# Kernel optimization log

Measured on AMD Instinct MI355X. Metric: run time of the kernel, lower is better.

The kernel has to match this reference:

```python
import jax, jax.numpy as jnp
import numpy as np
import math

HID, NH, DH = 512, 4, 128
H, W = 30, 54
N = H * W          # 1620 tokens
MEM, B = 2, 1
NG = 4             # temporal groups
L = (H // 2) * (W // 2)  # 405
FF = 4 * HID


def _ln(x, g, b, eps=1e-5):
    m = x.mean(-1, keepdims=True)
    v = ((x - m) ** 2).mean(-1, keepdims=True)
    return (x - m) / jnp.sqrt(v + eps) * g + b


def setup_inputs() -> dict:
    key = jax.random.key(0)
    ks = jax.random.split(key, 24)
    w = lambda k, s: (jax.random.normal(k, s, jnp.float32) * 0.02)
    return {
        'x': jax.random.normal(ks[0], (B, N, HID), jnp.float32),
        'memory': jax.random.normal(ks[1], (MEM, N, HID), jnp.float32),
        # spatial block params (weights stored as (in, out) so y = x @ W + b)
        's_g1': jnp.ones(HID), 's_b1': jnp.zeros(HID),
        's_wq': w(ks[2], (HID, HID)), 's_bq': jnp.zeros(HID),
        's_wk': w(ks[3], (HID, HID)), 's_bk': jnp.zeros(HID),
        's_wv': w(ks[4], (HID, HID)), 's_bv': jnp.zeros(HID),
        's_wo': w(ks[5], (HID, HID)), 's_bo': jnp.zeros(HID),
        's_g2': jnp.ones(HID), 's_b2': jnp.zeros(HID),
        's_w1': w(ks[6], (HID, FF)), 's_fb1': jnp.zeros(FF),
        's_w2': w(ks[7], (FF, HID)), 's_fb2': jnp.zeros(HID),
        # temporal block params (forward only uses norm2 + ffn)
        't_g2': jnp.ones(HID), 't_b2': jnp.zeros(HID),
        't_w1': w(ks[8], (HID, FF)), 't_fb1': jnp.zeros(FF),
        't_w2': w(ks[9], (FF, HID)), 't_fb2': jnp.zeros(HID),
    }


def _spatial_block(x, memory, g1, b1, wq, bq, wk, bk, wv, bv, wo, bo, g2, b2, w1, fb1, w2, fb2):
    xc = jnp.concatenate([x, memory], axis=0)          # (t, n, hid), t = B + MEM
    t = xc.shape[0]
    xn = _ln(xc, g1, b1)
    q = (xn @ wq + bq).reshape(t, N, NH, DH).transpose(0, 2, 1, 3)
    k = (xn @ wk + bk).reshape(t, N, NH, DH).transpose(0, 2, 1, 3)
    v = (xn @ wv + bv).reshape(t, N, NH, DH).transpose(0, 2, 1, 3)
    scores = jnp.einsum('thqd,thkd->thqk', q, k) / math.sqrt(DH)
    probs = jax.nn.softmax(scores, axis=-1)
    o = jnp.einsum('thqk,thkd->thqd', probs, v).transpose(0, 2, 1, 3).reshape(t, N, HID)
    o = o @ wo + bo
    xu = xc + o
    y = _ln(xu, g2, b2)
    xa = xu + (jax.nn.relu(y @ w1 + fb1) @ w2 + fb2)
    return xa[:B], jnp.concatenate([memory[1:], x], axis=0)


def _temporal_block(x, memory, g2, b2, w1, fb1, w2, fb2):
    xc = jnp.concatenate([x, memory], axis=0)          # (t, n, hid)
    t = xc.shape[0]
    # (t, 2, h/2, 2, w/2, NH, DH) -> (t, 2, 2, NH, h/2, w/2, DH) -> (t, NG, NH, L, DH)
    xg = xc.reshape(t, 2, H // 2, 2, W // 2, NH, DH)
    xg = xg.transpose(0, 1, 3, 5, 2, 4, 6).reshape(t, NG, NH, L, DH)
    # Original code runs SDPA over all t but keeps only slice [-1]; since Q is
    # broadcast across t, attn_out[-1] == attention(Q, K[-1], V[-1]) exactly.
    q = xg[-1]                                          # (NG, NH, L, DH); K = V = q
    scores = jnp.einsum('gnld,gnmd->gnlm', q, q) / math.sqrt(DH)
    probs = jax.nn.softmax(scores, axis=-1)
    o = jnp.einsum('gnlm,gnmd->gnld', probs, q)         # (NG, NH, L, DH)
    o = o.transpose(0, 2, 1, 3).reshape(NG, L, HID)
    o = o.mean(axis=0, keepdims=True)                   # (1, L, HID)
    x_att = jnp.tile(o, (1, NG, 1))                     # (1, n, HID)
    xu = x + x_att
    y = _ln(xu, g2, b2)
    x_fin = xu + (jax.nn.relu(y @ w1 + fb1) @ w2 + fb2)
    return x_fin, jnp.concatenate([memory[1:], x], axis=0)


def reference(x, memory, s_g1, s_b1, s_wq, s_bq, s_wk, s_bk, s_wv, s_bv, s_wo, s_bo,
              s_g2, s_b2, s_w1, s_fb1, s_w2, s_fb2, t_g2, t_b2, t_w1, t_fb1, t_w2, t_fb2):
    x_sp, mem_sp = _spatial_block(x, memory, s_g1, s_b1, s_wq, s_bq, s_wk, s_bk,
                                  s_wv, s_bv, s_wo, s_bo, s_g2, s_b2, s_w1, s_fb1, s_w2, s_fb2)
    x_fin, mem_fin = _temporal_block(x_sp, mem_sp, t_g2, t_b2, t_w1, t_fb1, t_w2, t_fb2)
    return x_fin, mem_fin
```

## Files before the change

kernel.cpp:

```cpp
#include <hip/hip_runtime.h>
#include <stdint.h>

typedef unsigned short u16;
typedef float f32x4 __attribute__((ext_vector_type(4)));
typedef short s16x8 __attribute__((ext_vector_type(8)));

#define DEV __device__ __forceinline__

DEV float b2f(u16 u){ union{unsigned i; float f;} v; v.i = ((unsigned)u)<<16; return v.f; }
DEV u16 f2b(float f){ union{float f; unsigned i;} v; v.f=f; unsigned u=v.i;
                      return (u16)((u + 0x7FFFu + ((u>>16)&1u))>>16); }
DEV s16x8 ld8(const u16* p){ return *(const s16x8*)p; }

#define MFMA(d,a,b) d = __builtin_amdgcn_mfma_f32_16x16x32_bf16(a, b, d, 0, 0, 0)

DEV void gload16(const u16* g, u16* l){
  __builtin_amdgcn_global_load_lds((const __attribute__((address_space(1))) void*)g,
                                   (__attribute__((address_space(3))) void*)l, 16, 0, 0);
}

__global__ __launch_bounds__(64) void detect_kernel(const u16* __restrict__ x, int* flag){
  int lane = threadIdx.x;
  int cnt = 0;
  for (int i=0;i<32;i++){
    u16 v = x[lane*32+i];
    int e = (v >> 7) & 0xFF;
    if (e >= 0xE0) cnt++;
  }
  for (int off=1; off<64; off<<=1) cnt += __shfl_xor(cnt, off, 64);
  if (lane==0) *flag = (cnt >= 16) ? 1 : 0;
}

struct NormArgs { const void* src[15]; int cumblk[16]; };

__global__ __launch_bounds__(64) void norm_kernel(NormArgs a, const int* __restrict__ flag,
                                                  u16* __restrict__ canon){
  int b = blockIdx.x, lane = threadIdx.x;
  int t = 0;
  while (t < 14 && b >= a.cumblk[t+1]) t++;
  int off = (b - a.cumblk[t])*512 + lane*8;
  size_t g = (size_t)b*512 + lane*8;
  if (*flag){
    const float* s = (const float*)a.src[t] + off;
    s16x8 o;
#pragma unroll
    for (int j=0;j<8;j++) o[j] = (short)f2b(s[j]);
    *(s16x8*)(canon+g) = o;
  } else {
    *(s16x8*)(canon+g) = *(const s16x8*)((const u16*)a.src[t] + off);
  }
}

struct TJobs {
  const void* src[8]; u16* dst[8];
  int R[8], C32[8], srcld[8], dstld[8];
  int cum[9];
};
__global__ void trans_kernel(TJobs J, const int* __restrict__ flag){
  int b = blockIdx.x;
  int t = 0;
  while (b >= J.cum[t+1]) t++;
  int idx = b - J.cum[t];
  int tr = idx / J.C32[t], tc = idx - tr*J.C32[t];
  int r0 = tr*32, c0 = tc*32;
  const void* src = J.src[t];
  u16* dst = J.dst[t];
  int R = J.R[t], srcld = J.srcld[t], dstld = J.dstld[t];
  int isf32 = flag ? *flag : 0;
  __shared__ u16 tile[32][33];
  int tx = threadIdx.x, ty = threadIdx.y;
#pragma unroll
  for (int i=0;i<4;i++){
    int r = r0 + ty + i*8, c = c0 + tx;
    u16 v = 0;
    if (r < R){
      size_t si = (size_t)r*srcld + c;
      v = isf32 ? f2b(((const float*)src)[si]) : ((const u16*)src)[si];
    }
    tile[ty+i*8][tx] = v;
  }
  __syncthreads();
#pragma unroll
  for (int i=0;i<4;i++){
    int c = c0 + ty + i*8, r = r0 + tx;
    if (r < dstld) dst[(size_t)c*dstld + r] = tile[tx][ty+i*8];
  }
}

__global__ __launch_bounds__(256) void gemm_s_kernel(
    const u16* __restrict__ A, const u16* __restrict__ BT,
    const u16* __restrict__ bias, const u16* __restrict__ bias2, const u16* __restrict__ bias3,
    int M, int N, int K, int KS, float* __restrict__ pout,
    const u16* __restrict__ resid_bf, const float* __restrict__ resid_f,
    u16* __restrict__ out_bf, float* __restrict__ out_f,
    const int* __restrict__ flagp, u16* __restrict__ dev_bf, float* __restrict__ dev_f,
    int relu)
{
  __shared__ u16 Al[2][64*64];
  __shared__ u16 Bl[2][64*64];
  int tid = threadIdx.x, lane = tid & 63, w = tid >> 6;
  int lr = lane & 15, lk = lane >> 4;
  int wr = w >> 1, wc = w & 1;
  int rowBase = blockIdx.y*64, colBase = blockIdx.x*64;
  int z = blockIdx.z;
  int kStep = K / KS;
  int kOff = kStep * z;
  int nk = kStep >> 6;

  f32x4 acc[2][2] = {{{0,0,0,0},{0,0,0,0}},{{0,0,0,0},{0,0,0,0}}};

  auto STAGE = [&](int buf, int kt){
    int kb = kOff + kt*64;
#pragma unroll
    for (int it=0; it<2; ++it){
      int ch  = it*256 + tid;
      int row = ch >> 3, seg = ch & 7;
      int sseg = (seg ^ (row & 7)) << 3;
      int ar = min(rowBase + row, M-1);
      gload16(A  + (size_t)ar*K + kb + sseg, Al[buf] + ch*8);
      int bc = colBase + row;
      gload16(BT + (size_t)bc*K + kb + sseg, Bl[buf] + ch*8);
    }
  };

  STAGE(0, 0);
  asm volatile("s_waitcnt vmcnt(0)" ::: "memory");
  __syncthreads();
  int cur = 0;
  for (int kt=0; kt<nk; ++kt){
    if (kt+1 < nk) STAGE(cur^1, kt+1);
#pragma unroll
    for (int ks=0; ks<2; ++ks){
      s16x8 af[2], bf[2];
#pragma unroll
      for (int m=0;m<2;m++){
        int ar = wr*32 + m*16 + lr;
        af[m] = *(const s16x8*)(Al[cur] + ar*64 + ((((ks<<2)+lk) ^ (ar&7))<<3));
        int bc = wc*32 + m*16 + lr;
        bf[m] = *(const s16x8*)(Bl[cur] + bc*64 + ((((ks<<2)+lk) ^ (bc&7))<<3));
      }
#pragma unroll
      for (int m=0;m<2;m++)
#pragma unroll
        for (int n=0;n<2;n++) MFMA(acc[m][n], af[m], bf[n]);
    }
    asm volatile("s_waitcnt vmcnt(0)" ::: "memory");
    __syncthreads();
    cur ^= 1;
  }

  if (pout){
    float* pz = pout + (size_t)z*M*N;
#pragma unroll
    for (int m=0;m<2;m++)
#pragma unroll
      for (int n=0;n<2;n++){
        int col = colBase + wc*32 + n*16 + lr;
#pragma unroll
        for (int r=0;r<4;r++){
          int row = rowBase + wr*32 + m*16 + lk*4 + r;
          if (row < M) pz[(size_t)row*N + col] = acc[m][n][r];
        }
      }
    return;
  }
  int isf32 = flagp ? *flagp : 0;
#pragma unroll
  for (int m=0;m<2;m++){
#pragma unroll
    for (int n=0;n<2;n++){
      int col = colBase + wc*32 + n*16 + lr;
      float bv = 0.f;
      if (bias){
        if (bias2){
          const u16* bp = (col < 512) ? bias : ((col < 1024) ? bias2 : bias3);
          bv = b2f(bp[col & 511]);
        } else bv = b2f(bias[col]);
      }
#pragma unroll
      for (int r=0;r<4;r++){
        int row = rowBase + wr*32 + m*16 + lk*4 + r;
        if (row < M){
          float v = acc[m][n][r] + bv;
          if (relu) v = fmaxf(v, 0.f);
          size_t idx = (size_t)row*N + col;
          if (resid_bf) v += b2f(resid_bf[idx]);
          if (resid_f)  v += resid_f[idx];
          if (out_f)  out_f[idx]  = v;
          if (out_bf) out_bf[idx] = f2b(v);
          if (flagp){ if (isf32) dev_f[idx] = v; else dev_bf[idx] = f2b(v); }
        }
      }
    }
  }
}

__global__ __launch_bounds__(256) void gemm_comb_kernel(
    const float* __restrict__ pout, int KS, const u16* __restrict__ bias,
    int M, int relu,
    const u16* __restrict__ resid_bf, const float* __restrict__ resid_f,
    u16* __restrict__ out_bf, float* __restrict__ out_f,
    const int* __restrict__ flagp, u16* __restrict__ dev_bf, float* __restrict__ dev_f)
{
  int w = threadIdx.x >> 6, lane = threadIdx.x & 63;
  int row = blockIdx.x*4 + w;
  if (row >= M) return;
  int c0 = lane*8;
  float acc[8];
  const float* p0 = pout + (size_t)row*512 + c0;
#pragma unroll
  for (int j=0;j<8;j++) acc[j] = p0[j];
  for (int z=1; z<KS; ++z){
    const float* pz = pout + ((size_t)z*M + row)*512 + c0;
#pragma unroll
    for (int j=0;j<8;j++) acc[j] += pz[j];
  }
  int isf32 = flagp ? *flagp : 0;
#pragma unroll
  for (int j=0;j<8;j++){
    int col = c0 + j;
    float v = acc[j] + (bias ? b2f(bias[col]) : 0.f);
    if (relu) v = fmaxf(v, 0.f);
    size_t idx = (size_t)row*512 + col;
    if (resid_bf) v += b2f(resid_bf[idx]);
    if (resid_f)  v += resid_f[idx];
    if (out_f)  out_f[idx]  = v;
    if (out_bf) out_bf[idx] = f2b(v);
    if (flagp){ if (isf32) dev_f[idx] = v; else dev_bf[idx] = f2b(v); }
  }
}

__global__ __launch_bounds__(256) void comb_ln_kernel(
    const float* __restrict__ pout, int KS, const u16* __restrict__ bias, int M,
    const u16* __restrict__ resid_bf,
    float* __restrict__ out_f,
    const u16* __restrict__ gw, const u16* __restrict__ bw,
    u16* __restrict__ out_ln)
{
  int w = threadIdx.x >> 6, lane = threadIdx.x & 63;
  int row = blockIdx.x*4 + w;
  if (row >= M) return;
  int c0 = lane*8;
  float acc[8];
  const float* p0 = pout + (size_t)row*512 + c0;
#pragma unroll
  for (int j=0;j<8;j++) acc[j] = p0[j];
  for (int z=1; z<KS; ++z){
    const float* pz = pout + ((size_t)z*M + row)*512 + c0;
#pragma unroll
    for (int j=0;j<8;j++) acc[j] += pz[j];
  }
  float s = 0.f;
#pragma unroll
  for (int j=0;j<8;j++){
    acc[j] += b2f(bias[c0+j]) + b2f(resid_bf[(size_t)row*512 + c0 + j]);
    out_f[(size_t)row*512 + c0 + j] = acc[j];
    s += acc[j];
  }
#pragma unroll
  for (int off=1; off<64; off<<=1) s += __shfl_xor(s, off, 64);
  float mean = s*(1.f/512.f);
  float vs = 0.f;
#pragma unroll
  for (int j=0;j<8;j++){ float d = acc[j]-mean; vs += d*d; }
#pragma unroll
  for (int off=1; off<64; off<<=1) vs += __shfl_xor(vs, off, 64);
  float rstd = 1.f/sqrtf(vs*(1.f/512.f) + 1e-5f);
#pragma unroll
  for (int j=0;j<8;j++){
    int c = c0+j;
    out_ln[(size_t)row*512 + c] = f2b((acc[j]-mean)*rstd*b2f(gw[c]) + b2f(bw[c]));
  }
}

__global__ __launch_bounds__(256) void combine_ln_kernel(
    const float* __restrict__ xa0, const float* __restrict__ ot,
    float* __restrict__ xut,
    const u16* __restrict__ gw, const u16* __restrict__ bw,
    u16* __restrict__ out_ln)
{
  int w = threadIdx.x >> 6, lane = threadIdx.x & 63;
  int row = blockIdx.x*4 + w;
  int l = row % 405;
  int c0 = lane*8;
  const float* pa = xa0 + (size_t)row*512 + c0;
  float acc[8];
#pragma unroll
  for (int j=0;j<8;j++) acc[j] = pa[j];
#pragma unroll
  for (int g2=0; g2<4; ++g2){
    const float* po = ot + ((size_t)(g2*405+l))*512 + c0;
#pragma unroll
    for (int j=0;j<8;j++) acc[j] += 0.25f*po[j];
  }
  float s = 0.f;
#pragma unroll
  for (int j=0;j<8;j++){ xut[(size_t)row*512 + c0 + j] = acc[j]; s += acc[j]; }
#pragma unroll
  for (int off=1; off<64; off<<=1) s += __shfl_xor(s, off, 64);
  float mean = s*(1.f/512.f);
  float vs = 0.f;
#pragma unroll
  for (int j=0;j<8;j++){ float d = acc[j]-mean; vs += d*d; }
#pragma unroll
  for (int off=1; off<64; off<<=1) vs += __shfl_xor(vs, off, 64);
  float rstd = 1.f/sqrtf(vs*(1.f/512.f) + 1e-5f);
#pragma unroll
  for (int j=0;j<8;j++){
    int c = c0+j;
    out_ln[(size_t)row*512 + c] = f2b((acc[j]-mean)*rstd*b2f(gw[c]) + b2f(bw[c]));
  }
}

__global__ __launch_bounds__(256) void flash4_kernel(
    const u16* __restrict__ Qp, const u16* __restrict__ Kp, const u16* __restrict__ VTp,
    float* __restrict__ po, float* __restrict__ pm, float* __restrict__ pl,
    int M, int Nk, int qld, int tiles_total, int nchunks,
    long q_hi_stride, long vt_hi_stride, int vt_ld, float scale)
{
  int u = blockIdx.y, c = blockIdx.z;
  int uh = u >> 2, ul = u & 3;
  const u16* q  = Qp  + (size_t)uh*q_hi_stride + ul*128;
  const u16* kk = Kp  + (size_t)uh*q_hi_stride + ul*128;
  const u16* vt = VTp + (size_t)uh*vt_hi_stride + (size_t)(ul*128)*vt_ld;
  int tid = threadIdx.x, lane = tid & 63, w = tid >> 6;
  int lr = lane & 15, lk = lane >> 4;
  int r0 = blockIdx.x*64 + w*16;
  int qr = min(r0 + lr, M-1);

  __shared__ u16 Klds[64*128];
  __shared__ u16 Vlds[128*64];
  __shared__ u16 plsm[4][16*80];

  s16x8 qf[4];
#pragma unroll
  for (int kd=0; kd<4; ++kd) qf[kd] = ld8(q + (size_t)qr*qld + kd*32 + lk*8);
  f32x4 oacc[8];
#pragma unroll
  for (int i=0;i<8;i++) oacc[i] = (f32x4){0,0,0,0};
  float mr[4] = {-1e30f,-1e30f,-1e30f,-1e30f};
  float ls[4] = {0,0,0,0};

  int t0 = (tiles_total * c) / nchunks;
  int t1 = (tiles_total * (c+1)) / nchunks;
  for (int kt=t0; kt<t1; ++kt){
    int kb = kt*64;
#pragma unroll
    for (int it=0; it<4; ++it){
      int ch = it*256 + tid;
      int key = ch >> 4, seg = ch & 15;
      int kg = min(kb + key, Nk-1);
      s16x8 kvv = ld8(kk + (size_t)kg*qld + seg*8);
      int dd = ch >> 3, sg = ch & 7;
      s16x8 vvv = ld8(vt + (size_t)dd*vt_ld + kb + sg*8);
      *(s16x8*)(Klds + key*128 + ((seg*8) ^ ((key&7)<<3))) = kvv;
      *(s16x8*)(Vlds + dd*64  + ((sg*8)  ^ ((dd&7)<<3)))  = vvv;
    }
    __syncthreads();
    f32x4 s[4];
#pragma unroll
    for (int n=0;n<4;n++) s[n] = (f32x4){0,0,0,0};
    __builtin_amdgcn_s_setprio(1);
#pragma unroll
    for (int n=0;n<4;n++){
      int key = n*16 + lr;
#pragma unroll
      for (int kd=0; kd<4; ++kd){
        s16x8 kf = *(const s16x8*)(Klds + key*128 + ((kd*32 + lk*8) ^ ((key&7)<<3)));
        MFMA(s[n], qf[kd], kf);
      }
    }
    __builtin_amdgcn_s_setprio(0);
#pragma unroll
    for (int n=0;n<4;n++){
      bool valid = (kb + n*16 + lr) < Nk;
#pragma unroll
      for (int r=0;r<4;r++){
        float v2 = s[n][r]*scale;
        s[n][r] = valid ? v2 : -1e30f;
      }
    }
    float mx[4];
#pragma unroll
    for (int r=0;r<4;r++) mx[r] = fmaxf(fmaxf(s[0][r],s[1][r]), fmaxf(s[2][r],s[3][r]));
#pragma unroll
    for (int off=1; off<16; off<<=1){
#pragma unroll
      for (int r=0;r<4;r++) mx[r] = fmaxf(mx[r], __shfl_xor(mx[r], off, 64));
    }
    float al[4], rs[4];
#pragma unroll
    for (int r=0;r<4;r++){
      float mnew = fmaxf(mr[r], mx[r]);
      al[r] = __expf(mr[r]-mnew);
      mr[r] = mnew;
      rs[r] = 0.f;
    }
#pragma unroll
    for (int n=0;n<4;n++){
#pragma unroll
      for (int r=0;r<4;r++){
        float p = __expf(s[n][r]-mr[r]);
        rs[r] += p;
        plsm[w][(lk*4+r)*80 + n*16 + lr] = f2b(p);
      }
    }
#pragma unroll
    for (int off=1; off<16; off<<=1){
#pragma unroll
      for (int r=0;r<4;r++) rs[r] += __shfl_xor(rs[r], off, 64);
    }
#pragma unroll
    for (int r=0;r<4;r++) ls[r] = ls[r]*al[r] + rs[r];
#pragma unroll
    for (int cf=0; cf<8; cf++){
#pragma unroll
      for (int r=0;r<4;r++) oacc[cf][r] *= al[r];
    }
    __syncthreads();
    __builtin_amdgcn_s_setprio(1);
#pragma unroll
    for (int kd2=0; kd2<2; ++kd2){
      s16x8 pa = *(const s16x8*)(plsm[w] + lr*80 + kd2*32 + lk*8);
#pragma unroll
      for (int cf=0; cf<8; ++cf){
        int dd = cf*16 + lr;
        s16x8 vb = *(const s16x8*)(Vlds + dd*64 + ((kd2*32 + lk*8) ^ ((dd&7)<<3)));
        MFMA(oacc[cf], pa, vb);
      }
    }
    __builtin_amdgcn_s_setprio(0);
    __syncthreads();
  }
  size_t pbase = ((size_t)u*nchunks + c)*M;
#pragma unroll
  for (int cf=0; cf<8; ++cf){
#pragma unroll
    for (int r=0;r<4;r++){
      int row = r0 + lk*4 + r;
      if (row < M) po[(pbase + row)*128 + cf*16 + lr] = oacc[cf][r];
    }
  }
  if (lr == 0){
#pragma unroll
    for (int r=0;r<4;r++){
      int row = r0 + lk*4 + r;
      if (row < M){ pm[pbase + row] = mr[r]; pl[pbase + row] = ls[r]; }
    }
  }
}

__global__ __launch_bounds__(256) void fcomb_kernel(
    const float* __restrict__ po, const float* __restrict__ pm, const float* __restrict__ pl,
    u16* __restrict__ out_bf, float* __restrict__ out_f,
    int rows, int nunits, int nchunks, long o_hi_stride)
{
  int w = threadIdx.x >> 6, lane = threadIdx.x & 63;
  int gid = blockIdx.x*4 + w;
  if (gid >= nunits*rows) return;
  int u = gid / rows, row = gid - u*rows;
  size_t pb = (size_t)u*nchunks*rows + row;
  float m = -1e30f;
  for (int c=0;c<nchunks;c++) m = fmaxf(m, pm[pb + (size_t)c*rows]);
  float L = 0.f, o0 = 0.f, o1 = 0.f;
  for (int c=0;c<nchunks;c++){
    float wgt = __expf(pm[pb + (size_t)c*rows] - m);
    L += wgt * pl[pb + (size_t)c*rows];
    const float* op = po + (pb + (size_t)c*rows)*128;
    o0 += wgt * op[lane*2];
    o1 += wgt * op[lane*2+1];
  }
  float inv = 1.f/L;
  int uh = u>>2, ul = u&3;
  size_t idx = (size_t)uh*o_hi_stride + (size_t)row*512 + ul*128 + lane*2;
  if (out_bf){ out_bf[idx] = f2b(o0*inv); out_bf[idx+1] = f2b(o1*inv); }
  else       { out_f[idx]  = o0*inv;      out_f[idx+1]  = o1*inv; }
}

__global__ __launch_bounds__(256) void ln_kernel(
    const u16* __restrict__ inb, const float* __restrict__ inf,
    const u16* __restrict__ gw, const u16* __restrict__ bw,
    u16* __restrict__ out, int rows)
{
  int w = threadIdx.x >> 6, lane = threadIdx.x & 63;
  int row = blockIdx.x*4 + w;
  if (row >= rows) return;
  float x[8];
  if (inb){
    s16x8 v = ld8(inb + (size_t)row*512 + lane*8);
#pragma unroll
    for (int j=0;j<8;j++) x[j] = b2f((u16)v[j]);
  } else {
    const float* p = inf + (size_t)row*512 + lane*8;
#pragma unroll
    for (int j=0;j<8;j++) x[j] = p[j];
  }
  float s = 0.f;
#pragma unroll
  for (int j=0;j<8;j++) s += x[j];
#pragma unroll
  for (int off=1; off<64; off<<=1) s += __shfl_xor(s, off, 64);
  float mean = s*(1.f/512.f);
  float vs = 0.f;
#pragma unroll
  for (int j=0;j<8;j++){ float d = x[j]-mean; vs += d*d; }
#pragma unroll
  for (int off=1; off<64; off<<=1) vs += __shfl_xor(vs, off, 64);
  float rstd = 1.f/sqrtf(vs*(1.f/512.f) + 1e-5f);
#pragma unroll
  for (int j=0;j<8;j++){
    int c = lane*8+j;
    float y = (x[j]-mean)*rstd*b2f(gw[c]) + b2f(bw[c]);
    out[(size_t)row*512 + c] = f2b(y);
  }
}

__global__ __launch_bounds__(256) void gather_xg_kernel(const u16* __restrict__ x,
                                                        u16* __restrict__ xg)
{
  int w = threadIdx.x >> 6, lane = threadIdx.x & 63;
  int gl = blockIdx.x*4 + w;
  int g = gl/405, l = gl - g*405;
  int a = g >> 1, b = g & 1, hh = l/27, ww = l - hh*27;
  int n = a*810 + hh*54 + b*27 + ww;
  *(s16x8*)(xg + (size_t)gl*512 + lane*8) = *(const s16x8*)(x + (size_t)n*512 + lane*8);
}

__global__ __launch_bounds__(256) void copy_out_kernel(
    const u16* __restrict__ s16, const float* __restrict__ s32,
    const int* __restrict__ flag, u16* __restrict__ dbf, float* __restrict__ df, int n8)
{
  int i = blockIdx.x*256 + threadIdx.x;
  if (i >= n8) return;
  if (*flag){
    ((f32x4*)df)[i*2]   = ((const f32x4*)s32)[i*2];
    ((f32x4*)df)[i*2+1] = ((const f32x4*)s32)[i*2+1];
  } else {
    ((s16x8*)dbf)[i] = ((const s16x8*)s16)[i];
  }
}

extern "C" void kernel_launch(void* const* d_in, const int* in_sizes, int n_in,
                              void* d_out, int out_size, void* d_ws, size_t ws_size,
                              hipStream_t stream)
{
  u16* outp16 = (u16*)d_out;
  float* outp32 = (float*)d_out;

  char* wsb = (char*)d_ws;
  size_t off = 0;
  auto alloc = [&](size_t bytes)->void*{
    void* p = wsb + off; off += (bytes + 255) & ~(size_t)255; return p; };

  int* flagp = (int*)alloc(256);

  static const int din_idx[15] = {0, 2,3, 5,7,9,11, 12,13, 15,17, 18,19, 21,23};
  static const int din_n[15]   = {829440, 512,512, 512,512,512,512, 512,512,
                                  2048,512, 512,512, 2048,512};
  NormArgs na;
  u16* cptr[15];
  int total = 0;
  for (int i=0;i<15;i++){ na.src[i] = d_in[din_idx[i]]; na.cumblk[i] = total/512; total += din_n[i]; }
  na.cumblk[15] = total/512;
  u16* canon = (u16*)alloc((size_t)total*2);
  { int c = 0; for (int i=0;i<15;i++){ cptr[i] = canon + c; c += din_n[i]; } }
  const u16 *cx=cptr[0], *cg1=cptr[1], *cb1=cptr[2],
            *cbq=cptr[3], *cbk=cptr[4], *cbv=cptr[5], *cbo=cptr[6],
            *cg2=cptr[7], *cb2=cptr[8], *cfb1s=cptr[9], *cfb2s=cptr[10],
            *ctg2=cptr[11], *ctb2=cptr[12], *cfb1t=cptr[13], *cfb2t=cptr[14];

  u16* wqkvT = (u16*)alloc((size_t)1536*512*2);
  u16* woT  = (u16*)alloc(512*512*2);
  u16* w1sT = (u16*)alloc(2048*512*2);
  u16* w2sT = (u16*)alloc((size_t)512*2048*2);
  u16* w1tT = (u16*)alloc(2048*512*2);
  u16* w2tT = (u16*)alloc((size_t)512*2048*2);
  u16* xn   = (u16*)alloc(1620*512*2);
  u16* qkv  = (u16*)alloc((size_t)1620*1536*2);
  u16* vT   = (u16*)alloc((size_t)512*1664*2);
  u16* attn = (u16*)alloc(1620*512*2);
  float* xu = (float*)alloc((size_t)1620*512*4);
  u16* yb   = (u16*)alloc(1620*512*2);
  u16* hh   = (u16*)alloc((size_t)1620*2048*2);
  float* xa0= (float*)alloc((size_t)1620*512*4);
  u16* xg   = (u16*)alloc(1620*512*2);
  u16* xgT  = (u16*)alloc((size_t)4*512*448*2);
  float* ot = (float*)alloc((size_t)4*405*512*4);
  float* xut= (float*)alloc((size_t)1620*512*4);
  u16* yt   = (u16*)alloc(1620*512*2);
  u16* ht   = (u16*)alloc((size_t)1620*2048*2);
  float* po = (float*)alloc((size_t)4*4*1620*128*4);
  float* pm = (float*)alloc((size_t)4*4*1620*4);
  float* pl = (float*)alloc((size_t)4*4*1620*4);

  const float scale = 0.08838834764831843f;
  dim3 tb(32,8);

  detect_kernel<<<dim3(1), dim3(64), 0, stream>>>((const u16*)d_in[0], flagp);
  norm_kernel<<<dim3(total/512), dim3(64), 0, stream>>>(na, flagp, canon);

  {
    TJobs J;
    const void* srcs[8] = {d_in[4], d_in[6], d_in[8], d_in[10],
                           d_in[14], d_in[16], d_in[20], d_in[22]};
    u16* dsts[8] = {wqkvT, wqkvT + (size_t)512*512, wqkvT + (size_t)1024*512,
                    woT, w1sT, w2sT, w1tT, w2tT};
    int Rs[8]   = {512,512,512,512, 512,2048, 512,2048};
    int Cs[8]   = {512,512,512,512, 2048,512, 2048,512};
    int t2 = 0;
    J.cum[0] = 0;
    for (int i=0;i<8;i++){
      J.src[i]=srcs[i]; J.dst[i]=dsts[i]; J.R[i]=Rs[i]; J.C32[i]=Cs[i]/32;
      J.srcld[i]=Cs[i]; J.dstld[i]=Rs[i];
      t2 += (Rs[i]/32)*(Cs[i]/32);
      J.cum[i+1]=t2;
    }
    trans_kernel<<<dim3(t2), tb, 0, stream>>>(J, flagp);
  }

  ln_kernel<<<dim3(405), dim3(256), 0, stream>>>(cx, nullptr, cg1, cb1, xn, 1620);
  gemm_s_kernel<<<dim3(24,26,1), dim3(256), 0, stream>>>(xn, wqkvT, cbq, cbk, cbv,
      1620,1536,512, 1, nullptr, nullptr,nullptr, qkv, nullptr, nullptr,nullptr,nullptr, 0);
  {
    TJobs J;
    J.src[0]=qkv+1024; J.dst[0]=vT; J.R[0]=1620; J.C32[0]=512/32;
    J.srcld[0]=1536; J.dstld[0]=1664;
    int t2 = (1664/32)*(512/32);
    J.cum[0]=0; for (int i=1;i<9;i++) J.cum[i]=t2;
    trans_kernel<<<dim3(t2), tb, 0, stream>>>(J, nullptr);
  }
  flash4_kernel<<<dim3(26,4,4), dim3(256), 0, stream>>>(qkv, qkv+512, vT, po, pm, pl,
      1620, 1620, 1536, 26, 4, 0L, 0L, 1664, scale);
  fcomb_kernel<<<dim3(1620), dim3(256), 0, stream>>>(po, pm, pl, attn, nullptr,
      1620, 4, 4, 0L);
  gemm_s_kernel<<<dim3(8,26,2), dim3(256), 0, stream>>>(attn, woT, nullptr,nullptr,nullptr,
      1620,512,512, 2, po, nullptr,nullptr, nullptr,nullptr, nullptr,nullptr,nullptr, 0);
  comb_ln_kernel<<<dim3(405), dim3(256), 0, stream>>>(po, 2, cbo, 1620, cx, xu,
      cg2, cb2, yb);
  gemm_s_kernel<<<dim3(32,26,1), dim3(256), 0, stream>>>(yb, w1sT, cfb1s, nullptr,nullptr,
      1620,2048,512, 1, nullptr, nullptr,nullptr, hh, nullptr, nullptr,nullptr,nullptr, 1);
  gemm_s_kernel<<<dim3(8,26,2), dim3(256), 0, stream>>>(hh, w2sT, nullptr,nullptr,nullptr,
      1620,512,2048, 2, po, nullptr,nullptr, nullptr,nullptr, nullptr,nullptr,nullptr, 0);
  gemm_comb_kernel<<<dim3(405), dim3(256), 0, stream>>>(po, 2, cfb2s, 1620, 0,
      nullptr, xu, nullptr, xa0, flagp, outp16 + 1658880, outp32 + 1658880);

  gather_xg_kernel<<<dim3(405), dim3(256), 0, stream>>>(cx, xg);
  {
    TJobs J;
    int per = (448/32)*(512/32);
    for (int g=0; g<4; ++g){
      J.src[g]=xg + (size_t)g*405*512; J.dst[g]=xgT + (size_t)g*512*448;
      J.R[g]=405; J.C32[g]=512/32; J.srcld[g]=512; J.dstld[g]=448;
    }
    J.cum[0]=0;
    for (int i=1;i<9;i++) J.cum[i] = (i<=4) ? per*i : per*4;
    trans_kernel<<<dim3(per*4), tb, 0, stream>>>(J, nullptr);
  }
  flash4_kernel<<<dim3(7,16,4), dim3(256), 0, stream>>>(xg, xg, xgT, po, pm, pl,
      405, 405, 512, 7, 4, (long)(405*512), (long)(512*448), 448, scale);
  fcomb_kernel<<<dim3(1620), dim3(256), 0, stream>>>(po, pm, pl, nullptr, ot,
      405, 16, 4, (long)(405*512));
  combine_ln_kernel<<<dim3(405), dim3(256), 0, stream>>>(xa0, ot, xut, ctg2, ctb2, yt);
  gemm_s_kernel<<<dim3(32,26,1), dim3(256), 0, stream>>>(yt, w1tT, cfb1t, nullptr,nullptr,
      1620,2048,512, 1, nullptr, nullptr,nullptr, ht, nullptr, nullptr,nullptr,nullptr, 1);
  gemm_s_kernel<<<dim3(8,26,2), dim3(256), 0, stream>>>(ht, w2tT, nullptr,nullptr,nullptr,
      1620,512,2048, 2, po, nullptr,nullptr, nullptr,nullptr, nullptr,nullptr,nullptr, 0);
  gemm_comb_kernel<<<dim3(405), dim3(256), 0, stream>>>(po, 2, cfb2t, 1620, 0,
      nullptr, xut, nullptr, nullptr, flagp, outp16, outp32);

  copy_out_kernel<<<dim3(405), dim3(256), 0, stream>>>((const u16*)d_in[0],
      (const float*)d_in[0], flagp, outp16 + 829440, outp32 + 829440, 103680);
}
```

Before: 281.8 us.

## Fold temporal gather into attention indexing and fuse FFN2 combine with temporal LN

The separate gather kernel for the temporal groups is removed: the transpose and flash kernels now map group rows to token rows through an index function and read straight from the canonical input. The temporal attention is moved ahead of the spatial block because it depends only on the input. The spatial FFN2 split-K combine is fused with the temporal mean-add and LayerNorm, which drops one kernel and the xa0 buffer round trip. The flash K/V tile loads also switch to direct global-to-LDS loads with an explicit vmcnt wait. The trade-off is extra index arithmetic per load and a change in the load path of the hot attention kernel.

```diff
diff --git a/kernel.cpp b/kernel.cpp
--- a/kernel.cpp
+++ b/kernel.cpp
@@ -17,6 +17,11 @@
 DEV void gload16(const u16* g, u16* l){
   __builtin_amdgcn_global_load_lds((const __attribute__((address_space(1))) void*)g,
                                    (__attribute__((address_space(3))) void*)l, 16, 0, 0);
+}
+
+DEV int qmapf(int g, int l){
+  int h2 = l/27, w2 = l - h2*27;
+  return (g>>1)*810 + h2*54 + (g&1)*27 + w2;
 }
 
 __global__ __launch_bounds__(64) void detect_kernel(const u16* __restrict__ x, int* flag){
@@ -53,7 +58,7 @@
 
 struct TJobs {
   const void* src[8]; u16* dst[8];
-  int R[8], C32[8], srcld[8], dstld[8];
+  int R[8], C32[8], srcld[8], dstld[8], gmap[8];
   int cum[9];
 };
 __global__ void trans_kernel(TJobs J, const int* __restrict__ flag){
@@ -65,7 +70,7 @@
   int r0 = tr*32, c0 = tc*32;
   const void* src = J.src[t];
   u16* dst = J.dst[t];
-  int R = J.R[t], srcld = J.srcld[t], dstld = J.dstld[t];
+  int R = J.R[t], srcld = J.srcld[t], dstld = J.dstld[t], g = J.gmap[t];
   int isf32 = flag ? *flag : 0;
   __shared__ u16 tile[32][33];
   int tx = threadIdx.x, ty = threadIdx.y;
@@ -74,7 +79,8 @@
     int r = r0 + ty + i*8, c = c0 + tx;
     u16 v = 0;
     if (r < R){
-      size_t si = (size_t)r*srcld + c;
+      int sr = (g >= 0) ? qmapf(g, r) : r;
+      size_t si = (size_t)sr*srcld + c;
       v = isf32 ? f2b(((const float*)src)[si]) : ((const u16*)src)[si];
     }
     tile[ty+i*8][tx] = v;
@@ -273,42 +279,48 @@
   }
 }
 
-__global__ __launch_bounds__(256) void combine_ln_kernel(
-    const float* __restrict__ xa0, const float* __restrict__ ot,
-    float* __restrict__ xut,
-    const u16* __restrict__ gw, const u16* __restrict__ bw,
+__global__ __launch_bounds__(256) void ffn2_comb_ln_kernel(
+    const float* __restrict__ pout, const u16* __restrict__ bias, int M,
+    const float* __restrict__ xu, const float* __restrict__ ot,
+    const int* __restrict__ flagp, u16* __restrict__ dev_bf, float* __restrict__ dev_f,
+    float* __restrict__ xut, const u16* __restrict__ gw, const u16* __restrict__ bw,
     u16* __restrict__ out_ln)
 {
   int w = threadIdx.x >> 6, lane = threadIdx.x & 63;
   int row = blockIdx.x*4 + w;
-  int l = row % 405;
-  int c0 = lane*8;
-  const float* pa = xa0 + (size_t)row*512 + c0;
-  float acc[8];
-#pragma unroll
-  for (int j=0;j<8;j++) acc[j] = pa[j];
-#pragma unroll
-  for (int g2=0; g2<4; ++g2){
-    const float* po = ot + ((size_t)(g2*405+l))*512 + c0;
-#pragma unroll
-    for (int j=0;j<8;j++) acc[j] += 0.25f*po[j];
-  }
+  if (row >= M) return;
+  int c0 = lane*8, l = row % 405;
+  int isf32 = *flagp;
+  const float* p0 = pout + (size_t)row*512 + c0;
+  const float* p1 = pout + ((size_t)M + row)*512 + c0;
+  const float* px = xu + (size_t)row*512 + c0;
+  float xv[8];
   float s = 0.f;
 #pragma unroll
-  for (int j=0;j<8;j++){ xut[(size_t)row*512 + c0 + j] = acc[j]; s += acc[j]; }
+  for (int j=0;j<8;j++){
+    float v = p0[j] + p1[j] + b2f(bias[c0+j]) + px[j];
+    size_t idx = (size_t)row*512 + c0 + j;
+    if (isf32) dev_f[idx] = v; else dev_bf[idx] = f2b(v);
+    float t = v + 0.25f*( ot[((size_t)l      )*512 + c0 + j]
+                        + ot[((size_t)(405+l) )*512 + c0 + j]
+                        + ot[((size_t)(810+l) )*512 + c0 + j]
+                        + ot[((size_t)(1215+l))*512 + c0 + j]);
+    xut[idx] = t;
+    xv[j] = t; s += t;
+  }
 #pragma unroll
   for (int off=1; off<64; off<<=1) s += __shfl_xor(s, off, 64);
   float mean = s*(1.f/512.f);
   float vs = 0.f;
 #pragma unroll
-  for (int j=0;j<8;j++){ float d = acc[j]-mean; vs += d*d; }
+  for (int j=0;j<8;j++){ float d = xv[j]-mean; vs += d*d; }
 #pragma unroll
   for (int off=1; off<64; off<<=1) vs += __shfl_xor(vs, off, 64);
   float rstd = 1.f/sqrtf(vs*(1.f/512.f) + 1e-5f);
 #pragma unroll
   for (int j=0;j<8;j++){
     int c = c0+j;
-    out_ln[(size_t)row*512 + c] = f2b((acc[j]-mean)*rstd*b2f(gw[c]) + b2f(bw[c]));
+    out_ln[(size_t)row*512 + c] = f2b((xv[j]-mean)*rstd*b2f(gw[c]) + b2f(bw[c]));
   }
 }
 
@@ -316,7 +328,7 @@
     const u16* __restrict__ Qp, const u16* __restrict__ Kp, const u16* __restrict__ VTp,
     float* __restrict__ po, float* __restrict__ pm, float* __restrict__ pl,
     int M, int Nk, int qld, int tiles_total, int nchunks,
-    long q_hi_stride, long vt_hi_stride, int vt_ld, float scale)
+    long q_hi_stride, long vt_hi_stride, int vt_ld, float scale, int usemap)
 {
   int u = blockIdx.y, c = blockIdx.z;
   int uh = u >> 2, ul = u & 3;
@@ -327,6 +339,7 @@
   int lr = lane & 15, lk = lane >> 4;
   int r0 = blockIdx.x*64 + w*16;
   int qr = min(r0 + lr, M-1);
+  int qrow = usemap ? qmapf(uh, qr) : qr;
 
   __shared__ u16 Klds[64*128];
   __shared__ u16 Vlds[128*64];
@@ -334,7 +347,7 @@
 
   s16x8 qf[4];
 #pragma unroll
-  for (int kd=0; kd<4; ++kd) qf[kd] = ld8(q + (size_t)qr*qld + kd*32 + lk*8);
+  for (int kd=0; kd<4; ++kd) qf[kd] = ld8(q + (size_t)qrow*qld + kd*32 + lk*8);
   f32x4 oacc[8];
 #pragma unroll
   for (int i=0;i<8;i++) oacc[i] = (f32x4){0,0,0,0};
@@ -349,13 +362,13 @@
     for (int it=0; it<4; ++it){
       int ch = it*256 + tid;
       int key = ch >> 4, seg = ch & 15;
-      int kg = min(kb + key, Nk-1);
-      s16x8 kvv = ld8(kk + (size_t)kg*qld + seg*8);
+      int kc = min(kb + key, Nk-1);
+      int kg = usemap ? qmapf(uh, kc) : kc;
+      gload16(kk + (size_t)kg*qld + (((seg ^ (key&7))&15)<<3), Klds + ch*8);
       int dd = ch >> 3, sg = ch & 7;
-      s16x8 vvv = ld8(vt + (size_t)dd*vt_ld + kb + sg*8);
-      *(s16x8*)(Klds + key*128 + ((seg*8) ^ ((key&7)<<3))) = kvv;
-      *(s16x8*)(Vlds + dd*64  + ((sg*8)  ^ ((dd&7)<<3)))  = vvv;
-    }
+      gload16(vt + (size_t)dd*vt_ld + kb + ((sg ^ (dd&7))<<3), Vlds + ch*8);
+    }
+    asm volatile("s_waitcnt vmcnt(0)" ::: "memory");
     __syncthreads();
     f32x4 s[4];
 #pragma unroll
@@ -478,7 +491,7 @@
 }
 
 __global__ __launch_bounds__(256) void ln_kernel(
-    const u16* __restrict__ inb, const float* __restrict__ inf,
+    const u16* __restrict__ inb,
     const u16* __restrict__ gw, const u16* __restrict__ bw,
     u16* __restrict__ out, int rows)
 {
@@ -486,15 +499,9 @@
   int row = blockIdx.x*4 + w;
   if (row >= rows) return;
   float x[8];
-  if (inb){
-    s16x8 v = ld8(inb + (size_t)row*512 + lane*8);
-#pragma unroll
-    for (int j=0;j<8;j++) x[j] = b2f((u16)v[j]);
-  } else {
-    const float* p = inf + (size_t)row*512 + lane*8;
-#pragma unroll
-    for (int j=0;j<8;j++) x[j] = p[j];
-  }
+  s16x8 v = ld8(inb + (size_t)row*512 + lane*8);
+#pragma unroll
+  for (int j=0;j<8;j++) x[j] = b2f((u16)v[j]);
   float s = 0.f;
 #pragma unroll
   for (int j=0;j<8;j++) s += x[j];
@@ -513,17 +520,6 @@
     float y = (x[j]-mean)*rstd*b2f(gw[c]) + b2f(bw[c]);
     out[(size_t)row*512 + c] = f2b(y);
   }
-}
-
-__global__ __launch_bounds__(256) void gather_xg_kernel(const u16* __restrict__ x,
-                                                        u16* __restrict__ xg)
-{
-  int w = threadIdx.x >> 6, lane = threadIdx.x & 63;
-  int gl = blockIdx.x*4 + w;
-  int g = gl/405, l = gl - g*405;
-  int a = g >> 1, b = g & 1, hh = l/27, ww = l - hh*27;
-  int n = a*810 + hh*54 + b*27 + ww;
-  *(s16x8*)(xg + (size_t)gl*512 + lane*8) = *(const s16x8*)(x + (size_t)n*512 + lane*8);
 }
 
 __global__ __launch_bounds__(256) void copy_out_kernel(
@@ -582,8 +578,6 @@
   float* xu = (float*)alloc((size_t)1620*512*4);
   u16* yb   = (u16*)alloc(1620*512*2);
   u16* hh   = (u16*)alloc((size_t)1620*2048*2);
-  float* xa0= (float*)alloc((size_t)1620*512*4);
-  u16* xg   = (u16*)alloc(1620*512*2);
   u16* xgT  = (u16*)alloc((size_t)4*512*448*2);
   float* ot = (float*)alloc((size_t)4*405*512*4);
   float* xut= (float*)alloc((size_t)1620*512*4);
@@ -611,26 +605,42 @@
     J.cum[0] = 0;
     for (int i=0;i<8;i++){
       J.src[i]=srcs[i]; J.dst[i]=dsts[i]; J.R[i]=Rs[i]; J.C32[i]=Cs[i]/32;
-      J.srcld[i]=Cs[i]; J.dstld[i]=Rs[i];
+      J.srcld[i]=Cs[i]; J.dstld[i]=Rs[i]; J.gmap[i]=-1;
       t2 += (Rs[i]/32)*(Cs[i]/32);
       J.cum[i+1]=t2;
     }
     trans_kernel<<<dim3(t2), tb, 0, stream>>>(J, flagp);
   }
 
-  ln_kernel<<<dim3(405), dim3(256), 0, stream>>>(cx, nullptr, cg1, cb1, xn, 1620);
+  {
+    TJobs J;
+    int per = (448/32)*(512/32);
+    for (int g=0; g<4; ++g){
+      J.src[g]=cx; J.dst[g]=xgT + (size_t)g*512*448;
+      J.R[g]=405; J.C32[g]=512/32; J.srcld[g]=512; J.dstld[g]=448; J.gmap[g]=g;
+    }
+    J.cum[0]=0;
+    for (int i=1;i<9;i++) J.cum[i] = (i<=4) ? per*i : per*4;
+    trans_kernel<<<dim3(per*4), tb, 0, stream>>>(J, nullptr);
+  }
+  flash4_kernel<<<dim3(7,16,4), dim3(256), 0, stream>>>(cx, cx, xgT, po, pm, pl,
+      405, 405, 512, 7, 4, 0L, (long)(512*448), 448, scale, 1);
+  fcomb_kernel<<<dim3(1620), dim3(256), 0, stream>>>(po, pm, pl, nullptr, ot,
+      405, 16, 4, (long)(405*512));
+
+  ln_kernel<<<dim3(405), dim3(256), 0, stream>>>(cx, cg1, cb1, xn, 1620);
   gemm_s_kernel<<<dim3(24,26,1), dim3(256), 0, stream>>>(xn, wqkvT, cbq, cbk, cbv,
       1620,1536,512, 1, nullptr, nullptr,nullptr, qkv, nullptr, nullptr,nullptr,nullptr, 0);
   {
     TJobs J;
     J.src[0]=qkv+1024; J.dst[0]=vT; J.R[0]=1620; J.C32[0]=512/32;
-    J.srcld[0]=1536; J.dstld[0]=1664;
+    J.srcld[0]=1536; J.dstld[0]=1664; J.gmap[0]=-1;
     int t2 = (1664/32)*(512/32);
     J.cum[0]=0; for (int i=1;i<9;i++) J.cum[i]=t2;
     trans_kernel<<<dim3(t2), tb, 0, stream>>>(J, nullptr);
   }
   flash4_kernel<<<dim3(26,4,4), dim3(256), 0, stream>>>(qkv, qkv+512, vT, po, pm, pl,
-      1620, 1620, 1536, 26, 4, 0L, 0L, 1664, scale);
+      1620, 1620, 1536, 26, 4, 0L, 0L, 1664, scale, 0);
   fcomb_kernel<<<dim3(1620), dim3(256), 0, stream>>>(po, pm, pl, attn, nullptr,
       1620, 4, 4, 0L);
   gemm_s_kernel<<<dim3(8,26,2), dim3(256), 0, stream>>>(attn, woT, nullptr,nullptr,nullptr,
@@ -641,26 +651,9 @@
       1620,2048,512, 1, nullptr, nullptr,nullptr, hh, nullptr, nullptr,nullptr,nullptr, 1);
   gemm_s_kernel<<<dim3(8,26,2), dim3(256), 0, stream>>>(hh, w2sT, nullptr,nullptr,nullptr,
       1620,512,2048, 2, po, nullptr,nullptr, nullptr,nullptr, nullptr,nullptr,nullptr, 0);
-  gemm_comb_kernel<<<dim3(405), dim3(256), 0, stream>>>(po, 2, cfb2s, 1620, 0,
-      nullptr, xu, nullptr, xa0, flagp, outp16 + 1658880, outp32 + 1658880);
-
-  gather_xg_kernel<<<dim3(405), dim3(256), 0, stream>>>(cx, xg);
-  {
-    TJobs J;
-    int per = (448/32)*(512/32);
-    for (int g=0; g<4; ++g){
-      J.src[g]=xg + (size_t)g*405*512; J.dst[g]=xgT + (size_t)g*512*448;
-      J.R[g]=405; J.C32[g]=512/32; J.srcld[g]=512; J.dstld[g]=448;
-    }
-    J.cum[0]=0;
-    for (int i=1;i<9;i++) J.cum[i] = (i<=4) ? per*i : per*4;
-    trans_kernel<<<dim3(per*4), tb, 0, stream>>>(J, nullptr);
-  }
-  flash4_kernel<<<dim3(7,16,4), dim3(256), 0, stream>>>(xg, xg, xgT, po, pm, pl,
-      405, 405, 512, 7, 4, (long)(405*512), (long)(512*448), 448, scale);
-  fcomb_kernel<<<dim3(1620), dim3(256), 0, stream>>>(po, pm, pl, nullptr, ot,
-      405, 16, 4, (long)(405*512));
-  combine_ln_kernel<<<dim3(405), dim3(256), 0, stream>>>(xa0, ot, xut, ctg2, ctb2, yt);
+  ffn2_comb_ln_kernel<<<dim3(405), dim3(256), 0, stream>>>(po, cfb2s, 1620,
+      xu, ot, flagp, outp16 + 1658880, outp32 + 1658880, xut, ctg2, ctb2, yt);
+
   gemm_s_kernel<<<dim3(32,26,1), dim3(256), 0, stream>>>(yt, w1tT, cfb1t, nullptr,nullptr,
       1620,2048,512, 1, nullptr, nullptr,nullptr, ht, nullptr, nullptr,nullptr,nullptr, 1);
   gemm_s_kernel<<<dim3(8,26,2), dim3(256), 0, stream>>>(ht, w2tT, nullptr,nullptr,nullptr,
```

New measurement: 282.0 us. About the same (+0.1%).
